# Optimization experiments

Measured on AMD Instinct MI355X. Metric: run time of the kernel, lower is better.

Reference implementation:

```python
import jax, jax.numpy as jnp
import numpy as np
from jax import lax

B, CIN, N = 4, 3, 2048
H, COUT, LEVELS = 128, 3, 3
HEADS = 8

# jnp.convolve(x, f, 'same') with len(f)=8 == correlation with f[::-1], x zero-padded (4,3).
# DWT then takes [::2], which is conv stride 2. IDWT zero-upsamples (lhs_dilation=2) then
# convolves 'same' with f[::-1], i.e. correlation with f, padding (4,4).

def _dwt(x, wlow, whigh):
    # x: (M, L) -> approx, detail each (M, L//2)
    rhs = jnp.stack([wlow[::-1], whigh[::-1]])[:, None, :]  # (2,1,8)
    out = lax.conv_general_dilated(x[:, None, :], rhs, window_strides=(2,),
                                   padding=[(4, 3)],
                                   dimension_numbers=('NCH', 'OIH', 'NCH'))
    return out[:, 0, :], out[:, 1, :]

def _idwt(a, d, wlow, whigh):
    # a, d: (M, L) -> (M, 2L); recon_low + recon_high fused as a 2-in-channel conv
    lhs = jnp.stack([a, d], axis=1)               # (M,2,L)
    rhs = jnp.stack([wlow, whigh])[None, :, :]    # (1,2,8)
    out = lax.conv_general_dilated(lhs, rhs, window_strides=(1,),
                                   padding=[(4, 4)], lhs_dilation=(2,),
                                   dimension_numbers=('NCH', 'OIH', 'NCH'))
    return out[:, 0, :]


def setup_inputs() -> dict:
    key = jax.random.key(0)
    ks = jax.random.split(key, 12)
    db4_low = jnp.array([0.23037781, 0.71484657, 0.63088076, -0.02798376,
                         -0.18703481, 0.03084138, 0.03288301, -0.0105974], jnp.float32)
    db4_high = jnp.array([-0.0105974, -0.03288301, 0.03084138, 0.18703481,
                          -0.02798376, -0.63088076, 0.71484657, -0.23037781], jnp.float32)
    def s(k, shape, fan_in):
        return jax.random.normal(k, shape, jnp.float32) * (1.0 / fan_in) ** 0.5
    return {
        'x': jax.random.normal(ks[0], (B, CIN, N), jnp.float32),
        'wlow': db4_low, 'whigh': db4_high,
        'Win': s(ks[1], (CIN, H), CIN), 'b_in': jnp.zeros((H,), jnp.float32),
        'W1': s(ks[2], (LEVELS, 2, 2 * H), 2), 'b1': jnp.zeros((LEVELS, 2 * H), jnp.float32),
        'W2': s(ks[3], (LEVELS, 2 * H, H), 2 * H), 'b2': jnp.zeros((LEVELS, H), jnp.float32),
        'Wq': s(ks[4], (H, H), H), 'bq': jnp.zeros((H,), jnp.float32),
        'Wk': s(ks[5], (H, H), H), 'bk': jnp.zeros((H,), jnp.float32),
        'Wv': s(ks[6], (H, H), H), 'bv': jnp.zeros((H,), jnp.float32),
        'Wo': s(ks[7], (H, H), H), 'bo': jnp.zeros((H,), jnp.float32),
        'Wout': s(ks[8], (H, COUT), H), 'bout': jnp.zeros((COUT,), jnp.float32),
    }


def reference(x, wlow, whigh, Win, b_in, W1, b1, W2, b2,
              Wq, bq, Wk, bk, Wv, bv, Wo, bo, Wout, bout):
    Bx = x.shape[0]
    # input projection: (B,CIN,N) -> (B,H,N)
    xp = jnp.einsum('bcn,ch->bhn', x, Win) + b_in[None, :, None]
    cur = xp.reshape(Bx * H, N)  # per-(batch,channel) 1D signals, fully batched
    proc = []  # processed coeffs per level; note approx == detail after the shared mean
    for lvl in range(LEVELS):
        a, d = _dwt(cur, wlow, whigh)                 # (M, L)
        c = jnp.stack([a, d], axis=-1)                # (M, L, 2)
        h = jax.nn.gelu(c @ W1[lvl] + b1[lvl])        # (M, L, 2H)
        p = (h @ W2[lvl] + b2[lvl]).mean(axis=-1)     # (M, L): mean over hidden dim
        proc.append(p)
        cur = a
    rec = proc[-1]  # start from deepest processed approx
    for lvl in range(LEVELS - 1, -1, -1):
        rec = _idwt(rec, proc[lvl], wlow, whigh)
    y = rec.reshape(Bx, H, N)
    # cross-level attention: standard MHA with embed_dim=H, 8 heads, no dropout
    seq = y.transpose(0, 2, 1)  # (B,N,H)
    dh = H // HEADS
    q = (seq @ Wq + bq).reshape(Bx, N, HEADS, dh)
    k = (seq @ Wk + bk).reshape(Bx, N, HEADS, dh)
    v = (seq @ Wv + bv).reshape(Bx, N, HEADS, dh)
    att = jnp.einsum('bqhd,bkhd->bhqk', q, k) * (dh ** -0.5)
    att = jax.nn.softmax(att, axis=-1)
    o = jnp.einsum('bhqk,bkhd->bqhd', att, v).reshape(Bx, N, H)
    o = o @ Wo + bo
    out = o @ Wout + bout  # (B,N,COUT)
    return out.transpose(0, 2, 1)  # (B,COUT,N)
```

## Files before the change

kernel.cpp:

```cpp
#include <hip/hip_runtime.h>

#define N_    2048
#define H_    128
#define B_    4
#define CIN_  3
#define COUT_ 3
#define LOG2E 1.44269504089f

__device__ __forceinline__ float gelu_tanh(float x) {
    float x2 = x * x;
    float e = __builtin_amdgcn_exp2f(x * fmaf(-0.10294340397f, x2, -2.30220899f));
    return x * __builtin_amdgcn_rcpf(1.0f + e);
}

__global__ void prep_kernel(const float* __restrict__ W1, const float* __restrict__ b1,
                            const float* __restrict__ W2, const float* __restrict__ b2,
                            const float* __restrict__ Wo, const float* __restrict__ bo,
                            const float* __restrict__ Wout, const float* __restrict__ bout,
                            float4* __restrict__ wpack, float* __restrict__ b2m,
                            float* __restrict__ wf, float* __restrict__ bf) {
    int gid = blockIdx.x * 256 + threadIdx.x;
    if (gid < 768) {
        const float* r = W2 + (size_t)gid * 128;
        float s = 0.f;
        for (int h = 0; h < 128; ++h) s += r[h];
        int lvl = gid >> 8, k = gid & 255;
        wpack[gid] = make_float4(W1[lvl * 512 + k], W1[lvl * 512 + 256 + k],
                                 b1[gid], s * (1.0f / 128.0f));
    } else if (gid < 771) {
        int lvl = gid - 768;
        const float* r = b2 + lvl * 128;
        float s = 0.f;
        for (int h = 0; h < 128; ++h) s += r[h];
        b2m[lvl] = s * (1.0f / 128.0f);
    } else if (gid >= 1024 && gid < 1408) {
        int e = gid - 1024;
        int h = e / 3, c = e - 3 * h;
        float s = 0.f;
        for (int j = 0; j < 128; ++j) s = fmaf(Wo[h * 128 + j], Wout[j * 3 + c], s);
        wf[e] = s;
    } else if (gid >= 1408 && gid < 1411) {
        int c = gid - 1408;
        float s = bout[c];
        for (int j = 0; j < 128; ++j) s = fmaf(bo[j], Wout[j * 3 + c], s);
        bf[c] = s;
    }
}

__global__ __launch_bounds__(256) void wavelet_fused_kernel(
        const float* __restrict__ x, const float* __restrict__ Win,
        const float* __restrict__ b_in,
        const float* __restrict__ wlow, const float* __restrict__ whigh,
        const float4* __restrict__ wpack, const float* __restrict__ b2m,
        float* __restrict__ r0g) {
    __shared__ float cur[2048];
    __shared__ float aA[1024];
    __shared__ float pp0[1024];
    __shared__ float aB[512];
    __shared__ float pp1[512];
    __shared__ float pp2[256];
    __shared__ float r2s[512];
    __shared__ float r1s[1024];
    int tid = threadIdx.x;
    int m = blockIdx.x;
    int b = m >> 7, h = m & 127;
    float w0 = Win[h], w1 = Win[128 + h], w2 = Win[256 + h];
    float bi = b_in[h];
    float wl[8], wh[8];
#pragma unroll
    for (int t = 0; t < 8; ++t) { wl[t] = wlow[t]; wh[t] = whigh[t]; }

    const float* xr = x + (size_t)b * (CIN_ * N_);
    for (int idx = tid; idx < 2048; idx += 256) {
        float v = bi;
        v = fmaf(xr[idx], w0, v);
        v = fmaf(xr[N_ + idx], w1, v);
        v = fmaf(xr[2 * N_ + idx], w2, v);
        cur[idx] = v;
    }
    __syncthreads();

    {
        float a4[4], d4[4], acc4[4];
#pragma unroll
        for (int u = 0; u < 4; ++u) {
            int i = tid + u * 256;
            int j0 = 2 * i - 4;
            float a = 0.f, d = 0.f;
#pragma unroll
            for (int t = 0; t < 8; ++t) {
                int j = j0 + t;
                float xv = ((unsigned)j < 2048u) ? cur[j] : 0.f;
                a = fmaf(xv, wl[7 - t], a);
                d = fmaf(xv, wh[7 - t], d);
            }
            a4[u] = a; d4[u] = d; aA[i] = a; acc4[u] = 0.f;
        }
#pragma unroll 4
        for (int kk = 0; kk < 256; ++kk) {
            float4 w = wpack[kk];
#pragma unroll
            for (int u = 0; u < 4; ++u) {
                float t = fmaf(a4[u], w.x, fmaf(d4[u], w.y, w.z));
                acc4[u] = fmaf(gelu_tanh(t), w.w, acc4[u]);
            }
        }
        float bb = b2m[0];
#pragma unroll
        for (int u = 0; u < 4; ++u) pp0[tid + u * 256] = acc4[u] + bb;
    }
    __syncthreads();

    {
        float a2v[2], d2v[2], acc2[2];
#pragma unroll
        for (int u = 0; u < 2; ++u) {
            int i = tid + u * 256;
            int j0 = 2 * i - 4;
            float a = 0.f, d = 0.f;
#pragma unroll
            for (int t = 0; t < 8; ++t) {
                int j = j0 + t;
                float xv = ((unsigned)j < 1024u) ? aA[j] : 0.f;
                a = fmaf(xv, wl[7 - t], a);
                d = fmaf(xv, wh[7 - t], d);
            }
            a2v[u] = a; d2v[u] = d; aB[i] = a; acc2[u] = 0.f;
        }
#pragma unroll 4
        for (int kk = 0; kk < 256; ++kk) {
            float4 w = wpack[256 + kk];
#pragma unroll
            for (int u = 0; u < 2; ++u) {
                float t = fmaf(a2v[u], w.x, fmaf(d2v[u], w.y, w.z));
                acc2[u] = fmaf(gelu_tanh(t), w.w, acc2[u]);
            }
        }
        float bb = b2m[1];
#pragma unroll
        for (int u = 0; u < 2; ++u) pp1[tid + u * 256] = acc2[u] + bb;
    }
    __syncthreads();

    {
        int j0 = 2 * tid - 4;
        float a = 0.f, d = 0.f;
#pragma unroll
        for (int t = 0; t < 8; ++t) {
            int j = j0 + t;
            float xv = ((unsigned)j < 512u) ? aB[j] : 0.f;
            a = fmaf(xv, wl[7 - t], a);
            d = fmaf(xv, wh[7 - t], d);
        }
        float acc = 0.f;
#pragma unroll 4
        for (int kk = 0; kk < 256; ++kk) {
            float4 w = wpack[512 + kk];
            float t = fmaf(a, w.x, fmaf(d, w.y, w.z));
            acc = fmaf(gelu_tanh(t), w.w, acc);
        }
        pp2[tid] = acc + b2m[2];
    }
    __syncthreads();

#pragma unroll
    for (int u = 0; u < 2; ++u) {
        int ii = tid + u * 256;
        int podd = ii & 1;
        int off0 = (ii >> 1) - 2 + podd;
        float r = 0.f;
#pragma unroll
        for (int s = 0; s < 4; ++s) {
            int idx = off0 + s;
            float av = ((unsigned)idx < 256u) ? pp2[idx] : 0.f;
            r = fmaf(av, wl[2 * s + podd] + wh[2 * s + podd], r);
        }
        r2s[ii] = r;
    }
    __syncthreads();

#pragma unroll
    for (int u = 0; u < 4; ++u) {
        int ii = tid + u * 256;
        int podd = ii & 1;
        int off0 = (ii >> 1) - 2 + podd;
        float r = 0.f;
#pragma unroll
        for (int s = 0; s < 4; ++s) {
            int idx = off0 + s;
            bool ok = (unsigned)idx < 512u;
            float av = ok ? r2s[idx] : 0.f;
            float dv = ok ? pp1[idx] : 0.f;
            r = fmaf(av, wl[2 * s + podd], r);
            r = fmaf(dv, wh[2 * s + podd], r);
        }
        r1s[ii] = r;
    }
    __syncthreads();

    float* orow = r0g + (size_t)m * 2048;
#pragma unroll
    for (int u = 0; u < 8; ++u) {
        int ii = tid + u * 256;
        int podd = ii & 1;
        int off0 = (ii >> 1) - 2 + podd;
        float r = 0.f;
#pragma unroll
        for (int s = 0; s < 4; ++s) {
            int idx = off0 + s;
            bool ok = (unsigned)idx < 1024u;
            float av = ok ? r1s[idx] : 0.f;
            float dv = ok ? pp0[idx] : 0.f;
            r = fmaf(av, wl[2 * s + podd], r);
            r = fmaf(dv, wh[2 * s + podd], r);
        }
        orow[ii] = r;
    }
}

__global__ __launch_bounds__(384) void qkv_kernel(
        const float* __restrict__ r0,
        const float* __restrict__ Wq, const float* __restrict__ bq,
        const float* __restrict__ Wk, const float* __restrict__ bk,
        const float* __restrict__ Wv, const float* __restrict__ bv,
        float* __restrict__ qB, float* __restrict__ kB, float* __restrict__ vB) {
    int tid = threadIdx.x;
    int rowbase = blockIdx.x * 16;
    int b  = rowbase >> 11;
    int n0 = rowbase & 2047;

    const float* W; const float* bias; float* dst; int jj;
    if (tid < 128)      { W = Wq; bias = bq; dst = qB; jj = tid; }
    else if (tid < 256) { W = Wk; bias = bk; dst = kB; jj = tid - 128; }
    else                { W = Wv; bias = bv; dst = vB; jj = tid - 256; }

    const float* abase = r0 + (size_t)b * (H_ * N_) + n0;
    float acc[16];
#pragma unroll
    for (int r = 0; r < 16; ++r) acc[r] = 0.f;
#pragma unroll 4
    for (int h = 0; h < 128; ++h) {
        float w = W[h * 128 + jj];
        const float* ar = abase + (size_t)h * N_;
#pragma unroll
        for (int r = 0; r < 16; ++r) acc[r] = fmaf(ar[r], w, acc[r]);
    }
    float bb = bias[jj];
    int head = jj >> 4, t = jj & 15;
    size_t obase = ((size_t)(b * 8 + head) * N_) * 16 + t;
#pragma unroll
    for (int r = 0; r < 16; ++r)
        dst[obase + (size_t)(n0 + r) * 16] = acc[r] + bb;
}

#define DOT4(acc, qq, aa) do { acc = fmaf(qq.x, aa.x, acc); acc = fmaf(qq.y, aa.y, acc); \
                               acc = fmaf(qq.z, aa.z, acc); acc = fmaf(qq.w, aa.w, acc); } while (0)
#define SCALE4(oo, c)     do { oo.x *= c; oo.y *= c; oo.z *= c; oo.w *= c; } while (0)
#define AXPY4(oo, p, aa)  do { oo.x = fmaf(p, aa.x, oo.x); oo.y = fmaf(p, aa.y, oo.y); \
                               oo.z = fmaf(p, aa.z, oo.z); oo.w = fmaf(p, aa.w, oo.w); } while (0)

template<int KS>
__global__ __launch_bounds__(128, 2) void attn_kernel(
        const float* __restrict__ qb, const float* __restrict__ kb,
        const float* __restrict__ vb,
        float* __restrict__ part_o, float* __restrict__ part_ml) {
    __shared__ float4 kt4[512];
    int tid   = threadIdx.x;
    int blk   = blockIdx.x;
    int split = blk % KS;
    int qblk  = (blk / KS) & 3;
    int bh    = blk / (4 * KS);

    const float4* ksrc = (const float4*)(kb + (size_t)bh * (N_ * 16));
    const float sc = 0.25f * LOG2E;

    float4 q[4][4];
    float  m[4], l[4];
    float4 o[4][4];
#pragma unroll
    for (int qi = 0; qi < 4; ++qi) {
        const float4* qr = (const float4*)(qb + ((size_t)bh * N_ + qblk * 512 + qi * 128 + tid) * 16);
#pragma unroll
        for (int j = 0; j < 4; ++j) { q[qi][j] = qr[j]; SCALE4(q[qi][j], sc); }
        m[qi] = -3.0e38f; l[qi] = 0.f;
#pragma unroll
        for (int j = 0; j < 4; ++j) o[qi][j] = make_float4(0.f, 0.f, 0.f, 0.f);
    }

    int k0 = split * (N_ / KS);
    for (int t0 = k0; t0 < k0 + N_ / KS; t0 += 128) {
        __syncthreads();
        const float4* ks = ksrc + t0 * 4;
#pragma unroll
        for (int u = 0; u < 4; ++u)
            kt4[tid + u * 128] = ks[tid + u * 128];
        __syncthreads();

        int tdiv = __shfl(t0, 0);
        const float4* vtile = (const float4*)(vb + (size_t)bh * (N_ * 16)) + (size_t)tdiv * 4;

        for (int c0 = 0; c0 < 128; c0 += 4) {
            float sv[4][4];
            float cm[4] = {-3.0e38f, -3.0e38f, -3.0e38f, -3.0e38f};
#pragma unroll
            for (int c = 0; c < 4; ++c) {
                int kr = (c0 + c) * 4;
                float4 k0v = kt4[kr], k1v = kt4[kr+1], k2v = kt4[kr+2], k3v = kt4[kr+3];
#pragma unroll
                for (int qi = 0; qi < 4; ++qi) {
                    float s0 = 0.f, s1 = 0.f;
                    DOT4(s0, q[qi][0], k0v); DOT4(s1, q[qi][1], k1v);
                    DOT4(s0, q[qi][2], k2v); DOT4(s1, q[qi][3], k3v);
                    sv[qi][c] = s0 + s1;
                    cm[qi] = fmaxf(cm[qi], sv[qi][c]);
                }
            }
            bool need = (cm[0] > m[0] + 8.f) || (cm[1] > m[1] + 8.f) ||
                        (cm[2] > m[2] + 8.f) || (cm[3] > m[3] + 8.f);
            if (__any(need)) {
#pragma unroll
                for (int qi = 0; qi < 4; ++qi) {
                    float mn = fmaxf(m[qi], cm[qi]);
                    float cr = __builtin_amdgcn_exp2f(m[qi] - mn);
                    l[qi] *= cr;
#pragma unroll
                    for (int j = 0; j < 4; ++j) SCALE4(o[qi][j], cr);
                    m[qi] = mn;
                }
            }
#pragma unroll
            for (int c = 0; c < 4; ++c) {
                int vr = (c0 + c) * 4;
                float4 v0 = vtile[vr], v1 = vtile[vr+1], v2 = vtile[vr+2], v3 = vtile[vr+3];
#pragma unroll
                for (int qi = 0; qi < 4; ++qi) {
                    float p = __builtin_amdgcn_exp2f(sv[qi][c] - m[qi]);
                    l[qi] += p;
                    AXPY4(o[qi][0], p, v0); AXPY4(o[qi][1], p, v1);
                    AXPY4(o[qi][2], p, v2); AXPY4(o[qi][3], p, v3);
                }
            }
        }
    }
#pragma unroll
    for (int qi = 0; qi < 4; ++qi) {
        int qg = bh * N_ + qblk * 512 + qi * 128 + tid;
        float4* po = (float4*)part_o + ((size_t)split * 65536 + qg) * 4;
        po[0] = o[qi][0]; po[1] = o[qi][1]; po[2] = o[qi][2]; po[3] = o[qi][3];
        ((float2*)part_ml)[(size_t)split * 65536 + qg] = make_float2(m[qi], l[qi]);
    }
}

template<int KS>
__global__ __launch_bounds__(128) void combine_final_kernel(
        const float* __restrict__ part_o, const float* __restrict__ part_ml,
        const float* __restrict__ wf, const float* __restrict__ bf,
        float* __restrict__ out) {
    __shared__ float ysh[16 * 129];
    int tid = threadIdx.x;
    int b = blockIdx.x >> 7, nb = blockIdx.x & 127;
    int head = tid >> 4, nl = tid & 15;
    int n = nb * 16 + nl;
    int qg = (b * 8 + head) * N_ + n;

    float m[KS], l[KS];
    float M = -3.0e38f;
#pragma unroll
    for (int s = 0; s < KS; ++s) {
        float2 ml = ((const float2*)part_ml)[(size_t)s * 65536 + qg];
        m[s] = ml.x; l[s] = ml.y;
        M = fmaxf(M, m[s]);
    }
    float w[KS], lt = 0.f;
#pragma unroll
    for (int s = 0; s < KS; ++s) {
        w[s] = __builtin_amdgcn_exp2f(m[s] - M);
        lt = fmaf(l[s], w[s], lt);
    }
    float inv = __builtin_amdgcn_rcpf(lt);
    float o[16];
#pragma unroll
    for (int j = 0; j < 16; ++j) o[j] = 0.f;
#pragma unroll
    for (int s = 0; s < KS; ++s) {
        const float4* po = (const float4*)part_o + ((size_t)s * 65536 + qg) * 4;
#pragma unroll
        for (int r = 0; r < 4; ++r) {
            float4 v = po[r];
            o[4*r+0] = fmaf(v.x, w[s], o[4*r+0]);
            o[4*r+1] = fmaf(v.y, w[s], o[4*r+1]);
            o[4*r+2] = fmaf(v.z, w[s], o[4*r+2]);
            o[4*r+3] = fmaf(v.w, w[s], o[4*r+3]);
        }
    }
    int col = head * 16;
#pragma unroll
    for (int j = 0; j < 16; ++j) ysh[nl * 129 + col + j] = o[j] * inv;
    __syncthreads();
    if (tid < 48) {
        int c = tid >> 4, nl2 = tid & 15;
        float acc = bf[c];
        const float* yr = ysh + nl2 * 129;
#pragma unroll 4
        for (int h = 0; h < 128; ++h) acc = fmaf(yr[h], wf[h * 3 + c], acc);
        out[((size_t)b * 3 + c) * N_ + nb * 16 + nl2] = acc;
    }
}

extern "C" void kernel_launch(void* const* d_in, const int* in_sizes, int n_in,
                              void* d_out, int out_size, void* d_ws, size_t ws_size,
                              hipStream_t stream) {
    const float* x    = (const float*)d_in[0];
    const float* wlow = (const float*)d_in[1];
    const float* whigh= (const float*)d_in[2];
    const float* Win  = (const float*)d_in[3];
    const float* b_in = (const float*)d_in[4];
    const float* W1   = (const float*)d_in[5];
    const float* b1   = (const float*)d_in[6];
    const float* W2   = (const float*)d_in[7];
    const float* b2   = (const float*)d_in[8];
    const float* Wq   = (const float*)d_in[9];
    const float* bq   = (const float*)d_in[10];
    const float* Wk   = (const float*)d_in[11];
    const float* bk   = (const float*)d_in[12];
    const float* Wv   = (const float*)d_in[13];
    const float* bv   = (const float*)d_in[14];
    const float* Wo   = (const float*)d_in[15];
    const float* bo   = (const float*)d_in[16];
    const float* Wout = (const float*)d_in[17];
    const float* bout = (const float*)d_in[18];
    float* out = (float*)d_out;
    (void)in_sizes; (void)n_in; (void)out_size;

    float* ws = (float*)d_ws;
    float* qBuf  = ws;
    float* kBuf  = ws + 1048576;
    float* vBuf  = ws + 2097152;
    float* base2 = ws + 3145728;
    float* r0    = base2;

    const size_t need16 = (3145728ull + 16ull * 1048576 + 16ull * 131072 + 4096ull) * 4;
    const size_t need8  = (3145728ull +  8ull * 1048576 +  8ull * 131072 + 4096ull) * 4;
    int KS = (ws_size >= need16) ? 16 : ((ws_size >= need8) ? 8 : 4);

    float* part_o  = base2;
    float* part_ml = base2 + (size_t)KS * 1048576;
    float* smalls  = part_ml + (size_t)KS * 131072;
    float4* wpack = (float4*)smalls;
    float* b2m = smalls + 3072;
    float* wf  = smalls + 3088;
    float* bf  = smalls + 3472;

    prep_kernel<<<8, 256, 0, stream>>>(W1, b1, W2, b2, Wo, bo, Wout, bout, wpack, b2m, wf, bf);

    wavelet_fused_kernel<<<512, 256, 0, stream>>>(x, Win, b_in, wlow, whigh,
                                                  wpack, b2m, r0);

    qkv_kernel<<<512, 384, 0, stream>>>(r0, Wq, bq, Wk, bk, Wv, bv, qBuf, kBuf, vBuf);

    if (KS == 16) {
        attn_kernel<16><<<32 * 4 * 16, 128, 0, stream>>>(qBuf, kBuf, vBuf, part_o, part_ml);
        combine_final_kernel<16><<<512, 128, 0, stream>>>(part_o, part_ml, wf, bf, out);
    } else if (KS == 8) {
        attn_kernel<8><<<32 * 4 * 8, 128, 0, stream>>>(qBuf, kBuf, vBuf, part_o, part_ml);
        combine_final_kernel<8><<<512, 128, 0, stream>>>(part_o, part_ml, wf, bf, out);
    } else {
        attn_kernel<4><<<32 * 4 * 4, 128, 0, stream>>>(qBuf, kBuf, vBuf, part_o, part_ml);
        combine_final_kernel<4><<<512, 128, 0, stream>>>(part_o, part_ml, wf, bf, out);
    }
}
```

Baseline: 364.6 us.

## Widen wavelet blocks, split qkv rows, stage V in LDS, wave-reduce prep

The prep kernel now gives each reduction to one wavefront and sums with shuffles instead of a serial loop per thread. The wavelet kernel moves to 512 threads per block, and the level-2 MLP's hidden units are split between two thread halves and then summed through shared memory. qkv_kernel handles 8 rows per block instead of 16, doubling the grid. The attention kernel stages V tiles in LDS next to K instead of reading them from global memory. These target low parallelism in the serial stages and global V reads, at the cost of more LDS and an extra sync.

Result: faster. 339.6 us (-6.9%).

```diff
diff --git a/kernel.cpp b/kernel.cpp
--- a/kernel.cpp
+++ b/kernel.cpp
@@ -13,41 +13,49 @@
     return x * __builtin_amdgcn_rcpf(1.0f + e);
 }
 
-__global__ void prep_kernel(const float* __restrict__ W1, const float* __restrict__ b1,
-                            const float* __restrict__ W2, const float* __restrict__ b2,
-                            const float* __restrict__ Wo, const float* __restrict__ bo,
-                            const float* __restrict__ Wout, const float* __restrict__ bout,
-                            float4* __restrict__ wpack, float* __restrict__ b2m,
-                            float* __restrict__ wf, float* __restrict__ bf) {
-    int gid = blockIdx.x * 256 + threadIdx.x;
-    if (gid < 768) {
-        const float* r = W2 + (size_t)gid * 128;
-        float s = 0.f;
-        for (int h = 0; h < 128; ++h) s += r[h];
-        int lvl = gid >> 8, k = gid & 255;
-        wpack[gid] = make_float4(W1[lvl * 512 + k], W1[lvl * 512 + 256 + k],
-                                 b1[gid], s * (1.0f / 128.0f));
-    } else if (gid < 771) {
-        int lvl = gid - 768;
+__device__ __forceinline__ float wave_sum(float s) {
+#pragma unroll
+    for (int off = 32; off; off >>= 1) s += __shfl_xor(s, off);
+    return s;
+}
+
+__global__ __launch_bounds__(256) void prep_kernel(
+        const float* __restrict__ W1, const float* __restrict__ b1,
+        const float* __restrict__ W2, const float* __restrict__ b2,
+        const float* __restrict__ Wo, const float* __restrict__ bo,
+        const float* __restrict__ Wout, const float* __restrict__ bout,
+        float4* __restrict__ wpack, float* __restrict__ b2m,
+        float* __restrict__ wf, float* __restrict__ bf) {
+    int wid  = (blockIdx.x * 256 + threadIdx.x) >> 6;
+    int lane = threadIdx.x & 63;
+    if (wid < 768) {
+        const float* r = W2 + (size_t)wid * 128;
+        float s = wave_sum(r[lane] + r[lane + 64]);
+        if (lane == 0) {
+            int lvl = wid >> 8, k = wid & 255;
+            wpack[wid] = make_float4(W1[lvl * 512 + k], W1[lvl * 512 + 256 + k],
+                                     b1[wid], s * (1.0f / 128.0f));
+        }
+    } else if (wid < 771) {
+        int lvl = wid - 768;
         const float* r = b2 + lvl * 128;
-        float s = 0.f;
-        for (int h = 0; h < 128; ++h) s += r[h];
-        b2m[lvl] = s * (1.0f / 128.0f);
-    } else if (gid >= 1024 && gid < 1408) {
-        int e = gid - 1024;
+        float s = wave_sum(r[lane] + r[lane + 64]);
+        if (lane == 0) b2m[lvl] = s * (1.0f / 128.0f);
+    } else if (wid < 1155) {
+        int e = wid - 771;
         int h = e / 3, c = e - 3 * h;
-        float s = 0.f;
-        for (int j = 0; j < 128; ++j) s = fmaf(Wo[h * 128 + j], Wout[j * 3 + c], s);
-        wf[e] = s;
-    } else if (gid >= 1408 && gid < 1411) {
-        int c = gid - 1408;
-        float s = bout[c];
-        for (int j = 0; j < 128; ++j) s = fmaf(bo[j], Wout[j * 3 + c], s);
-        bf[c] = s;
-    }
-}
-
-__global__ __launch_bounds__(256) void wavelet_fused_kernel(
+        float s = wave_sum(fmaf(Wo[h * 128 + lane], Wout[lane * 3 + c],
+                                Wo[h * 128 + 64 + lane] * Wout[(lane + 64) * 3 + c]));
+        if (lane == 0) wf[e] = s;
+    } else if (wid < 1158) {
+        int c = wid - 1155;
+        float s = wave_sum(fmaf(bo[lane], Wout[lane * 3 + c],
+                                bo[lane + 64] * Wout[(lane + 64) * 3 + c]));
+        if (lane == 0) bf[c] = s + bout[c];
+    }
+}
+
+__global__ __launch_bounds__(512) void wavelet_fused_kernel(
         const float* __restrict__ x, const float* __restrict__ Win,
         const float* __restrict__ b_in,
         const float* __restrict__ wlow, const float* __restrict__ whigh,
@@ -71,7 +79,7 @@
     for (int t = 0; t < 8; ++t) { wl[t] = wlow[t]; wh[t] = whigh[t]; }
 
     const float* xr = x + (size_t)b * (CIN_ * N_);
-    for (int idx = tid; idx < 2048; idx += 256) {
+    for (int idx = tid; idx < 2048; idx += 512) {
         float v = bi;
         v = fmaf(xr[idx], w0, v);
         v = fmaf(xr[N_ + idx], w1, v);
@@ -81,10 +89,10 @@
     __syncthreads();
 
     {
-        float a4[4], d4[4], acc4[4];
-#pragma unroll
-        for (int u = 0; u < 4; ++u) {
-            int i = tid + u * 256;
+        float a2[2], d2[2], acc2[2];
+#pragma unroll
+        for (int u = 0; u < 2; ++u) {
+            int i = tid + u * 512;
             int j0 = 2 * i - 4;
             float a = 0.f, d = 0.f;
 #pragma unroll
@@ -94,56 +102,50 @@
                 a = fmaf(xv, wl[7 - t], a);
                 d = fmaf(xv, wh[7 - t], d);
             }
-            a4[u] = a; d4[u] = d; aA[i] = a; acc4[u] = 0.f;
+            a2[u] = a; d2[u] = d; aA[i] = a; acc2[u] = 0.f;
         }
 #pragma unroll 4
         for (int kk = 0; kk < 256; ++kk) {
             float4 w = wpack[kk];
 #pragma unroll
-            for (int u = 0; u < 4; ++u) {
-                float t = fmaf(a4[u], w.x, fmaf(d4[u], w.y, w.z));
-                acc4[u] = fmaf(gelu_tanh(t), w.w, acc4[u]);
+            for (int u = 0; u < 2; ++u) {
+                float t = fmaf(a2[u], w.x, fmaf(d2[u], w.y, w.z));
+                acc2[u] = fmaf(gelu_tanh(t), w.w, acc2[u]);
             }
         }
         float bb = b2m[0];
 #pragma unroll
-        for (int u = 0; u < 4; ++u) pp0[tid + u * 256] = acc4[u] + bb;
+        for (int u = 0; u < 2; ++u) pp0[tid + u * 512] = acc2[u] + bb;
     }
     __syncthreads();
 
     {
-        float a2v[2], d2v[2], acc2[2];
-#pragma unroll
-        for (int u = 0; u < 2; ++u) {
-            int i = tid + u * 256;
-            int j0 = 2 * i - 4;
-            float a = 0.f, d = 0.f;
-#pragma unroll
-            for (int t = 0; t < 8; ++t) {
-                int j = j0 + t;
-                float xv = ((unsigned)j < 1024u) ? aA[j] : 0.f;
-                a = fmaf(xv, wl[7 - t], a);
-                d = fmaf(xv, wh[7 - t], d);
-            }
-            a2v[u] = a; d2v[u] = d; aB[i] = a; acc2[u] = 0.f;
-        }
+        int i = tid;
+        int j0 = 2 * i - 4;
+        float a = 0.f, d = 0.f;
+#pragma unroll
+        for (int t = 0; t < 8; ++t) {
+            int j = j0 + t;
+            float xv = ((unsigned)j < 1024u) ? aA[j] : 0.f;
+            a = fmaf(xv, wl[7 - t], a);
+            d = fmaf(xv, wh[7 - t], d);
+        }
+        aB[i] = a;
+        float acc = 0.f;
 #pragma unroll 4
         for (int kk = 0; kk < 256; ++kk) {
             float4 w = wpack[256 + kk];
-#pragma unroll
-            for (int u = 0; u < 2; ++u) {
-                float t = fmaf(a2v[u], w.x, fmaf(d2v[u], w.y, w.z));
-                acc2[u] = fmaf(gelu_tanh(t), w.w, acc2[u]);
-            }
-        }
-        float bb = b2m[1];
-#pragma unroll
-        for (int u = 0; u < 2; ++u) pp1[tid + u * 256] = acc2[u] + bb;
+            float t = fmaf(a, w.x, fmaf(d, w.y, w.z));
+            acc = fmaf(gelu_tanh(t), w.w, acc);
+        }
+        pp1[i] = acc + b2m[1];
     }
     __syncthreads();
 
     {
-        int j0 = 2 * tid - 4;
+        int i    = tid & 255;
+        int half = tid >> 8;
+        int j0 = 2 * i - 4;
         float a = 0.f, d = 0.f;
 #pragma unroll
         for (int t = 0; t < 8; ++t) {
@@ -153,19 +155,21 @@
             d = fmaf(xv, wh[7 - t], d);
         }
         float acc = 0.f;
+        int kb = half * 128;
 #pragma unroll 4
-        for (int kk = 0; kk < 256; ++kk) {
-            float4 w = wpack[512 + kk];
+        for (int kk = 0; kk < 128; ++kk) {
+            float4 w = wpack[512 + kb + kk];
             float t = fmaf(a, w.x, fmaf(d, w.y, w.z));
             acc = fmaf(gelu_tanh(t), w.w, acc);
         }
-        pp2[tid] = acc + b2m[2];
-    }
-    __syncthreads();
-
-#pragma unroll
-    for (int u = 0; u < 2; ++u) {
-        int ii = tid + u * 256;
+        r1s[tid] = acc;
+    }
+    __syncthreads();
+    if (tid < 256) pp2[tid] = r1s[tid] + r1s[tid + 256] + b2m[2];
+    __syncthreads();
+
+    {
+        int ii = tid;
         int podd = ii & 1;
         int off0 = (ii >> 1) - 2 + podd;
         float r = 0.f;
@@ -180,8 +184,8 @@
     __syncthreads();
 
 #pragma unroll
-    for (int u = 0; u < 4; ++u) {
-        int ii = tid + u * 256;
+    for (int u = 0; u < 2; ++u) {
+        int ii = tid + u * 512;
         int podd = ii & 1;
         int off0 = (ii >> 1) - 2 + podd;
         float r = 0.f;
@@ -200,8 +204,8 @@
 
     float* orow = r0g + (size_t)m * 2048;
 #pragma unroll
-    for (int u = 0; u < 8; ++u) {
-        int ii = tid + u * 256;
+    for (int u = 0; u < 4; ++u) {
+        int ii = tid + u * 512;
         int podd = ii & 1;
         int off0 = (ii >> 1) - 2 + podd;
         float r = 0.f;
@@ -225,7 +229,7 @@
         const float* __restrict__ Wv, const float* __restrict__ bv,
         float* __restrict__ qB, float* __restrict__ kB, float* __restrict__ vB) {
     int tid = threadIdx.x;
-    int rowbase = blockIdx.x * 16;
+    int rowbase = blockIdx.x * 8;
     int b  = rowbase >> 11;
     int n0 = rowbase & 2047;
 
@@ -235,21 +239,21 @@
     else                { W = Wv; bias = bv; dst = vB; jj = tid - 256; }
 
     const float* abase = r0 + (size_t)b * (H_ * N_) + n0;
-    float acc[16];
-#pragma unroll
-    for (int r = 0; r < 16; ++r) acc[r] = 0.f;
+    float acc[8];
+#pragma unroll
+    for (int r = 0; r < 8; ++r) acc[r] = 0.f;
 #pragma unroll 4
     for (int h = 0; h < 128; ++h) {
         float w = W[h * 128 + jj];
         const float* ar = abase + (size_t)h * N_;
 #pragma unroll
-        for (int r = 0; r < 16; ++r) acc[r] = fmaf(ar[r], w, acc[r]);
+        for (int r = 0; r < 8; ++r) acc[r] = fmaf(ar[r], w, acc[r]);
     }
     float bb = bias[jj];
     int head = jj >> 4, t = jj & 15;
     size_t obase = ((size_t)(b * 8 + head) * N_) * 16 + t;
 #pragma unroll
-    for (int r = 0; r < 16; ++r)
+    for (int r = 0; r < 8; ++r)
         dst[obase + (size_t)(n0 + r) * 16] = acc[r] + bb;
 }
 
@@ -265,6 +269,7 @@
         const float* __restrict__ vb,
         float* __restrict__ part_o, float* __restrict__ part_ml) {
     __shared__ float4 kt4[512];
+    __shared__ float4 vt4[512];
     int tid   = threadIdx.x;
     int blk   = blockIdx.x;
     int split = blk % KS;
@@ -272,6 +277,7 @@
     int bh    = blk / (4 * KS);
 
     const float4* ksrc = (const float4*)(kb + (size_t)bh * (N_ * 16));
+    const float4* vsrc = (const float4*)(vb + (size_t)bh * (N_ * 16));
     const float sc = 0.25f * LOG2E;
 
     float4 q[4][4];
@@ -291,13 +297,13 @@
     for (int t0 = k0; t0 < k0 + N_ / KS; t0 += 128) {
         __syncthreads();
         const float4* ks = ksrc + t0 * 4;
-#pragma unroll
-        for (int u = 0; u < 4; ++u)
+        const float4* vs = vsrc + t0 * 4;
+#pragma unroll
+        for (int u = 0; u < 4; ++u) {
             kt4[tid + u * 128] = ks[tid + u * 128];
+            vt4[tid + u * 128] = vs[tid + u * 128];
+        }
         __syncthreads();
-
-        int tdiv = __shfl(t0, 0);
-        const float4* vtile = (const float4*)(vb + (size_t)bh * (N_ * 16)) + (size_t)tdiv * 4;
 
         for (int c0 = 0; c0 < 128; c0 += 4) {
             float sv[4][4];
@@ -331,7 +337,7 @@
 #pragma unroll
             for (int c = 0; c < 4; ++c) {
                 int vr = (c0 + c) * 4;
-                float4 v0 = vtile[vr], v1 = vtile[vr+1], v2 = vtile[vr+2], v3 = vtile[vr+3];
+                float4 v0 = vt4[vr], v1 = vt4[vr+1], v2 = vt4[vr+2], v3 = vt4[vr+3];
 #pragma unroll
                 for (int qi = 0; qi < 4; ++qi) {
                     float p = __builtin_amdgcn_exp2f(sv[qi][c] - m[qi]);
@@ -451,12 +457,12 @@
     float* wf  = smalls + 3088;
     float* bf  = smalls + 3472;
 
-    prep_kernel<<<8, 256, 0, stream>>>(W1, b1, W2, b2, Wo, bo, Wout, bout, wpack, b2m, wf, bf);
-
-    wavelet_fused_kernel<<<512, 256, 0, stream>>>(x, Win, b_in, wlow, whigh,
+    prep_kernel<<<290, 256, 0, stream>>>(W1, b1, W2, b2, Wo, bo, Wout, bout, wpack, b2m, wf, bf);
+
+    wavelet_fused_kernel<<<512, 512, 0, stream>>>(x, Win, b_in, wlow, whigh,
                                                   wpack, b2m, r0);
 
-    qkv_kernel<<<512, 384, 0, stream>>>(r0, Wq, bq, Wk, bk, Wv, bv, qBuf, kBuf, vBuf);
+    qkv_kernel<<<1024, 384, 0, stream>>>(r0, Wq, bq, Wk, bk, Wv, bv, qBuf, kBuf, vBuf);
 
     if (KS == 16) {
         attn_kernel<16><<<32 * 4 * 16, 128, 0, stream>>>(qBuf, kBuf, vBuf, part_o, part_ml);
```
